# Performance work log

Measured on AMD Instinct MI355X. Metric: run time of the kernel, lower is better.

Reference implementation:

```python
import jax, jax.numpy as jnp
import numpy as np

EMBED_DIM = 64  # scale factor dim (matches head dim)


def setup_inputs() -> dict:
    key0 = jax.random.key(0)
    kq, kk, kv = jax.random.split(key0, 3)
    shape = (2, 16, 2048, 64)  # [B, H, S, D]
    return {
        "query": jax.random.normal(kq, shape, dtype=jnp.float32),
        "key": jax.random.normal(kk, shape, dtype=jnp.float32),
        "value": jax.random.normal(kv, shape, dtype=jnp.float32),
    }


def reference(query, key, value):
    # qk = Q K^T / sqrt(embed_dim); softmax over last dim; @ V
    inv_scale = jnp.sqrt(jnp.asarray(EMBED_DIM, dtype=query.dtype))
    scores = jnp.einsum("bhqd,bhkd->bhqk", query, key) / inv_scale
    probs = jax.nn.softmax(scores, axis=-1)
    # dropout_p=0.0 -> identity (eval semantics)
    return jnp.einsum("bhqk,bhkd->bhqd", probs, value)
```

## Files before the change

kernel.cpp:

```cpp
#include <hip/hip_runtime.h>
#include <hip/hip_bf16.h>

#define S_LEN 2048
#define DDIM  64
#define NT    (S_LEN / 64)
#define SCALE  0.125f
#define SCALE2 0.18033688f
#define NELEM  4194304
#define NQROW  65536
#define WC_LGKM0 0xc07f

#if __has_builtin(__builtin_amdgcn_permlane32_swap) && __has_builtin(__builtin_amdgcn_permlane16_swap)
#define HAVE_PLSWAP 1
#else
#define HAVE_PLSWAP 0
#endif

typedef __attribute__((ext_vector_type(8))) short short8;
typedef __attribute__((ext_vector_type(4))) float floatx4;
typedef __attribute__((ext_vector_type(2))) float floatx2;
typedef __attribute__((ext_vector_type(2))) __bf16 bf16x2;

__device__ __forceinline__ short f2bf(float f) {
    union { float f; unsigned u; } v; v.f = f;
    return (short)((v.u + 0x7fffu + ((v.u >> 16) & 1u)) >> 16);
}

__device__ __forceinline__ unsigned pk2bf(float a, float b) {
    floatx2 f; f[0] = a; f[1] = b;
    bf16x2 h = __builtin_convertvector(f, bf16x2);
    union { bf16x2 v; unsigned u; } c; c.v = h; return c.u;
}

__device__ __forceinline__ float fexp2(float x) {
#if __has_builtin(__builtin_amdgcn_exp2f)
    return __builtin_amdgcn_exp2f(x);
#else
    return exp2f(x);
#endif
}

#if HAVE_PLSWAP
__device__ __forceinline__ void plswap32(unsigned &a, unsigned &b) {
    auto r = __builtin_amdgcn_permlane32_swap((int)a, (int)b, false, false);
    a = (unsigned)r[0]; b = (unsigned)r[1];
}
__device__ __forceinline__ void plswap16(unsigned &a, unsigned &b) {
    auto r = __builtin_amdgcn_permlane16_swap((int)a, (int)b, false, false);
    a = (unsigned)r[0]; b = (unsigned)r[1];
}
#endif

__global__ __launch_bounds__(256) void prep_kv(const float* __restrict__ K,
                                               const float* __restrict__ V,
                                               short* __restrict__ Kb,
                                               short* __restrict__ Vt) {
    const int bh = blockIdx.x & 31;
    const int st = blockIdx.x >> 5;
    const int t  = threadIdx.x;
    const size_t tile_off = (size_t)bh * (S_LEN * DDIM) + (size_t)st * (64 * DDIM);

    {
        const float* src = K + tile_off + t * 16;
        short* dst = Kb + tile_off + t * 16;
        #pragma unroll
        for (int h = 0; h < 2; ++h) {
            float4 a = *(const float4*)(src + h * 8);
            float4 b = *(const float4*)(src + h * 8 + 4);
            uint4 o;
            o.x = pk2bf(a.x, a.y); o.y = pk2bf(a.z, a.w);
            o.z = pk2bf(b.x, b.y); o.w = pk2bf(b.z, b.w);
            *(uint4*)(dst + h * 8) = o;
        }
    }

    {
        const int s4 = (t & 15) * 4;
        const int d4 = (t >> 4) * 4;
        const float* src = V + tile_off;
        float4 v0 = *(const float4*)(src + (size_t)(s4 + 0) * 64 + d4);
        float4 v1 = *(const float4*)(src + (size_t)(s4 + 1) * 64 + d4);
        float4 v2 = *(const float4*)(src + (size_t)(s4 + 2) * 64 + d4);
        float4 v3 = *(const float4*)(src + (size_t)(s4 + 3) * 64 + d4);
        const float* r0 = (const float*)&v0;
        const float* r1 = (const float*)&v1;
        const float* r2 = (const float*)&v2;
        const float* r3 = (const float*)&v3;
        short* dstb = Vt + (size_t)bh * (DDIM * S_LEN) + (size_t)st * 64 + s4;
        #pragma unroll
        for (int dd = 0; dd < 4; ++dd) {
            uint2 o;
            o.x = pk2bf(r0[dd], r1[dd]);
            o.y = pk2bf(r2[dd], r3[dd]);
            *(uint2*)(dstb + (size_t)(d4 + dd) * S_LEN) = o;
        }
    }
}

__global__ __launch_bounds__(512) void attn_sm8(
    const float* __restrict__ Q, const short* __restrict__ Kb,
    const short* __restrict__ Vt, float* __restrict__ O)
{
    __shared__ short Ks[2][64 * 64];
    __shared__ short Vs[2][64 * 64];
    __shared__ float Dl[128];
#if !HAVE_PLSWAP
    __shared__ short Pl[8][32 * 64];
#endif

    constexpr int NIT = NT / 2;

    const int tid  = threadIdx.x;
    const int wave = tid >> 6;
    const int grp  = wave >> 2;
    const int w4   = wave & 3;
    const int lane = tid & 63;
    const int l16  = lane & 15;
    const int quad = lane >> 4;
    const int x7   = l16 & 7;

    const int bh = blockIdx.x & 31;
    const int qt = blockIdx.x >> 5;
    const int ks = grp;
    const size_t base = (size_t)bh * (S_LEN * DDIM);

    const int g   = tid & 255;
    const int ci0 = g,        r0 = ci0 >> 3, c0 = (ci0 & 7) ^ (r0 & 7);
    const int ci1 = 256 + g,  r1 = ci1 >> 3, c1 = (ci1 & 7) ^ (r1 & 7);
    const size_t koff = (size_t)ks * NIT * (64 * 64);
    const size_t voff = (size_t)ks * NIT * 64;
    const short* pK0 = Kb + base + koff + r0 * 64 + c0 * 8;
    const short* pK1 = Kb + base + koff + r1 * 64 + c1 * 8;
    const short* pV0 = Vt + base + voff + (size_t)r0 * S_LEN + c0 * 8;
    const short* pV1 = Vt + base + voff + (size_t)r1 * S_LEN + c1 * 8;

    short8 rk0 = *(const short8*)pK0;
    short8 rk1 = *(const short8*)pK1;
    short8 rv0 = *(const short8*)pV0;
    short8 rv1 = *(const short8*)pV1;

    short8 qf[2][2];
    #pragma unroll
    for (int nq = 0; nq < 2; ++nq) {
        const float* qp = Q + base + (size_t)(qt * 128 + w4 * 32 + nq * 16 + l16) * 64 + quad * 8;
        #pragma unroll
        for (int kt = 0; kt < 2; ++kt) {
            float4 a = *(const float4*)(qp + kt * 32);
            float4 b = *(const float4*)(qp + kt * 32 + 4);
            union { unsigned u[4]; short8 s; } qc;
            qc.u[0] = pk2bf(a.x * SCALE2, a.y * SCALE2);
            qc.u[1] = pk2bf(a.z * SCALE2, a.w * SCALE2);
            qc.u[2] = pk2bf(b.x * SCALE2, b.y * SCALE2);
            qc.u[3] = pk2bf(b.z * SCALE2, b.w * SCALE2);
            qf[nq][kt] = qc.s;
        }
    }

    floatx4 oacc[2][4];
    float rs[2];
    #pragma unroll
    for (int mt = 0; mt < 2; ++mt) {
        #pragma unroll
        for (int dt = 0; dt < 4; ++dt) oacc[mt][dt] = (floatx4){0.f,0.f,0.f,0.f};
        rs[mt] = 0.f;
    }

    short* Ksg = &Ks[grp][0];
    short* Vsg = &Vs[grp][0];
#if !HAVE_PLSWAP
    short* Pw = &Pl[wave][0];
#endif

    for (int kb = 0; kb < NIT; ++kb) {
        if (kb) __builtin_amdgcn_s_barrier();

        *(short8*)&Ksg[ci0 * 8] = rk0;
        *(short8*)&Ksg[ci1 * 8] = rk1;
        *(short8*)&Vsg[ci0 * 8] = rv0;
        *(short8*)&Vsg[ci1 * 8] = rv1;

        if (kb + 1 < NIT) {
            const int ok = (kb + 1) * (64 * 64), ov = (kb + 1) * 64;
            rk0 = *(const short8*)(pK0 + ok);
            rk1 = *(const short8*)(pK1 + ok);
            rv0 = *(const short8*)(pV0 + ov);
            rv1 = *(const short8*)(pV1 + ov);
        }

        __builtin_amdgcn_s_waitcnt(WC_LGKM0);
        __builtin_amdgcn_s_barrier();

        floatx4 sc[2][4];
        #pragma unroll
        for (int mk = 0; mk < 4; ++mk) {
            floatx4 a0 = (floatx4){0.f,0.f,0.f,0.f};
            floatx4 a1 = (floatx4){0.f,0.f,0.f,0.f};
            #pragma unroll
            for (int kt = 0; kt < 2; ++kt) {
                const int csw = (kt * 4 + quad) ^ x7;
                short8 kf = *(const short8*)&Ksg[(mk * 16 + l16) * 64 + csw * 8];
                a0 = __builtin_amdgcn_mfma_f32_16x16x32_bf16(kf, qf[0][kt], a0, 0, 0, 0);
                a1 = __builtin_amdgcn_mfma_f32_16x16x32_bf16(kf, qf[1][kt], a1, 0, 0, 0);
            }
            sc[0][mk] = a0; sc[1][mk] = a1;
        }

#if HAVE_PLSWAP
        unsigned pa[2][4], pb[2][4];
        #pragma unroll
        for (int nq = 0; nq < 2; ++nq) {
            #pragma unroll
            for (int mk = 0; mk < 4; ++mk) {
                float p0 = fexp2(sc[nq][mk][0]);
                float p1 = fexp2(sc[nq][mk][1]);
                float p2 = fexp2(sc[nq][mk][2]);
                float p3 = fexp2(sc[nq][mk][3]);
                rs[nq] += (p0 + p1) + (p2 + p3);
                pa[nq][mk] = pk2bf(p0, p1);
                pb[nq][mk] = pk2bf(p2, p3);
            }
        }

        #pragma unroll
        for (int kt = 0; kt < 2; ++kt) {
            short8 pf[2];
            #pragma unroll
            for (int nq = 0; nq < 2; ++nq) {
                unsigned a0 = pa[nq][2 * kt], a1 = pa[nq][2 * kt + 1];
                unsigned b0 = pb[nq][2 * kt], b1 = pb[nq][2 * kt + 1];
                plswap32(a0, a1); plswap16(a0, a1);
                plswap32(b0, b1); plswap16(b0, b1);
                union { unsigned u[4]; short8 s; } c;
                c.u[0] = a0; c.u[1] = b0; c.u[2] = a1; c.u[3] = b1;
                pf[nq] = c.s;
            }
            const int csw = (kt * 4 + quad) ^ x7;
            #pragma unroll
            for (int dt = 0; dt < 4; ++dt) {
                short8 vf = *(const short8*)&Vsg[(dt * 16 + l16) * 64 + csw * 8];
                oacc[0][dt] = __builtin_amdgcn_mfma_f32_16x16x32_bf16(pf[0], vf, oacc[0][dt], 0, 0, 0);
                oacc[1][dt] = __builtin_amdgcn_mfma_f32_16x16x32_bf16(pf[1], vf, oacc[1][dt], 0, 0, 0);
            }
        }
#else
        #pragma unroll
        for (int nq = 0; nq < 2; ++nq) {
            const int prow = (nq * 16 + l16) * 64;
            #pragma unroll
            for (int mk = 0; mk < 4; ++mk) {
                float p0 = fexp2(sc[nq][mk][0]);
                float p1 = fexp2(sc[nq][mk][1]);
                float p2 = fexp2(sc[nq][mk][2]);
                float p3 = fexp2(sc[nq][mk][3]);
                rs[nq] += (p0 + p1) + (p2 + p3);
                uint2 pv; pv.x = pk2bf(p0, p1); pv.y = pk2bf(p2, p3);
                const int c8 = (mk * 4 + quad) ^ (2 * x7);
                *(uint2*)&Pw[prow + c8 * 4] = pv;
            }
        }
        #pragma unroll
        for (int kt = 0; kt < 2; ++kt) {
            const int csw = (kt * 4 + quad) ^ x7;
            short8 pf0 = *(const short8*)&Pw[(l16)      * 64 + csw * 8];
            short8 pf1 = *(const short8*)&Pw[(16 + l16) * 64 + csw * 8];
            #pragma unroll
            for (int dt = 0; dt < 4; ++dt) {
                short8 vf = *(const short8*)&Vsg[(dt * 16 + l16) * 64 + csw * 8];
                oacc[0][dt] = __builtin_amdgcn_mfma_f32_16x16x32_bf16(pf0, vf, oacc[0][dt], 0, 0, 0);
                oacc[1][dt] = __builtin_amdgcn_mfma_f32_16x16x32_bf16(pf1, vf, oacc[1][dt], 0, 0, 0);
            }
        }
#endif
    }

    float sred[2];
    #pragma unroll
    for (int nq = 0; nq < 2; ++nq) {
        float s = rs[nq];
        s += __shfl_xor(s, 16, 64);
        s += __shfl_xor(s, 32, 64);
        sred[nq] = s;
    }

    if (grp == 1 && quad == 0) {
        Dl[w4 * 32 + l16]      = sred[0];
        Dl[w4 * 32 + 16 + l16] = sred[1];
    }
    __syncthreads();

    float invt[2];
    if (grp == 0) {
        invt[0] = 1.0f / (sred[0] + Dl[w4 * 32 + l16]);
        invt[1] = 1.0f / (sred[1] + Dl[w4 * 32 + 16 + l16]);
    }

    float* Nb = (float*)&Ks[0][0];
    #pragma unroll
    for (int mt = 0; mt < 2; ++mt) {
        if (grp == 1) {
            #pragma unroll
            for (int dt = 0; dt < 4; ++dt)
                #pragma unroll
                for (int r = 0; r < 4; ++r)
                    Nb[(dt * 4 + r) * 256 + w4 * 64 + lane] = oacc[mt][dt][r];
        }
        __syncthreads();
        if (grp == 0) {
            #pragma unroll
            for (int r = 0; r < 4; ++r) {
                const int row = qt * 128 + w4 * 32 + mt * 16 + quad * 4 + r;
                const float it = __shfl(invt[mt], quad * 4 + r, 64);
                float* op = O + base + (size_t)row * 64 + l16;
                #pragma unroll
                for (int dt = 0; dt < 4; ++dt)
                    op[dt * 16] = (oacc[mt][dt][r] + Nb[(dt * 4 + r) * 256 + w4 * 64 + lane]) * it;
            }
        }
        __syncthreads();
    }
}

#define BQ    64
#define BKEY  64
#define KPAD  72

__global__ __launch_bounds__(256) void attn_kernel(
    const float* __restrict__ Q, const float* __restrict__ K,
    const float* __restrict__ V, float* __restrict__ O)
{
    __shared__ short Ksh[BKEY * KPAD];
    __shared__ short Vtt[DDIM * KPAD];
    __shared__ short Pls[4][16 * KPAD];

    const int tid  = threadIdx.x;
    const int wave = tid >> 6;
    const int lane = tid & 63;
    const int l16  = lane & 15;
    const int quad = lane >> 4;

    const int bh = blockIdx.x & 31;
    const int qt = blockIdx.x >> 5;
    const size_t base = (size_t)bh * S_LEN * DDIM;

    const int qrow = qt * BQ + wave * 16 + l16;
    short8 qf[2];
    {
        const float* qp = Q + base + (size_t)qrow * DDIM + quad * 8;
        #pragma unroll
        for (int kt = 0; kt < 2; ++kt) {
            float4 a = *(const float4*)(qp + kt * 32);
            float4 b = *(const float4*)(qp + kt * 32 + 4);
            short* d = (short*)&qf[kt];
            d[0]=f2bf(a.x*SCALE); d[1]=f2bf(a.y*SCALE); d[2]=f2bf(a.z*SCALE); d[3]=f2bf(a.w*SCALE);
            d[4]=f2bf(b.x*SCALE); d[5]=f2bf(b.y*SCALE); d[6]=f2bf(b.z*SCALE); d[7]=f2bf(b.w*SCALE);
        }
    }

    float m_i[4], l_i[4];
    floatx4 oacc[4];
    #pragma unroll
    for (int r = 0; r < 4; ++r) { m_i[r] = -3.0e38f; l_i[r] = 0.f; }
    #pragma unroll
    for (int dt = 0; dt < 4; ++dt) oacc[dt] = (floatx4){0.f, 0.f, 0.f, 0.f};

    const int skey = tid >> 2;
    const int scol = (tid & 3) * 4;

    for (int kb = 0; kb < S_LEN / BKEY; ++kb) {
        const float* Kg = K + base + (size_t)kb * BKEY * DDIM + (size_t)skey * DDIM;
        const float* Vg = V + base + (size_t)kb * BKEY * DDIM + (size_t)skey * DDIM;
        #pragma unroll
        for (int i = 0; i < 4; ++i) {
            const int c = scol + i * 16;
            float4 kv = *(const float4*)(Kg + c);
            short* kd = &Ksh[skey * KPAD + c];
            kd[0]=f2bf(kv.x); kd[1]=f2bf(kv.y); kd[2]=f2bf(kv.z); kd[3]=f2bf(kv.w);
            float4 vv = *(const float4*)(Vg + c);
            Vtt[(c+0)*KPAD + skey] = f2bf(vv.x);
            Vtt[(c+1)*KPAD + skey] = f2bf(vv.y);
            Vtt[(c+2)*KPAD + skey] = f2bf(vv.z);
            Vtt[(c+3)*KPAD + skey] = f2bf(vv.w);
        }
        __syncthreads();

        floatx4 sc[4];
        #pragma unroll
        for (int nt = 0; nt < 4; ++nt) {
            floatx4 acc = (floatx4){0.f, 0.f, 0.f, 0.f};
            #pragma unroll
            for (int kt = 0; kt < 2; ++kt) {
                short8 kf = *(const short8*)&Ksh[(nt*16 + l16) * KPAD + kt*32 + quad*8];
                acc = __builtin_amdgcn_mfma_f32_16x16x32_bf16(qf[kt], kf, acc, 0, 0, 0);
            }
            sc[nt] = acc;
        }

        short* Pw = &Pls[wave][0];
        #pragma unroll
        for (int r = 0; r < 4; ++r) {
            float mx = fmaxf(fmaxf(sc[0][r], sc[1][r]), fmaxf(sc[2][r], sc[3][r]));
            #pragma unroll
            for (int off = 1; off < 16; off <<= 1)
                mx = fmaxf(mx, __shfl_xor(mx, off, 64));
            const float mnew  = fmaxf(m_i[r], mx);
            const float alpha = __expf(m_i[r] - mnew);
            m_i[r] = mnew;
            float rsum = 0.f;
            #pragma unroll
            for (int nt = 0; nt < 4; ++nt) {
                float p = __expf(sc[nt][r] - mnew);
                rsum += p;
                Pw[(quad*4 + r) * KPAD + nt*16 + l16] = f2bf(p);
            }
            #pragma unroll
            for (int off = 1; off < 16; off <<= 1)
                rsum += __shfl_xor(rsum, off, 64);
            l_i[r] = l_i[r] * alpha + rsum;
            oacc[0][r] *= alpha; oacc[1][r] *= alpha;
            oacc[2][r] *= alpha; oacc[3][r] *= alpha;
        }

        #pragma unroll
        for (int kt = 0; kt < 2; ++kt) {
            short8 pf = *(const short8*)&Pw[l16 * KPAD + kt*32 + quad*8];
            #pragma unroll
            for (int dt = 0; dt < 4; ++dt) {
                short8 vf = *(const short8*)&Vtt[(dt*16 + l16) * KPAD + kt*32 + quad*8];
                oacc[dt] = __builtin_amdgcn_mfma_f32_16x16x32_bf16(pf, vf, oacc[dt], 0, 0, 0);
            }
        }
        __syncthreads();
    }

    #pragma unroll
    for (int r = 0; r < 4; ++r) {
        const float inv = 1.0f / l_i[r];
        const int row = qt * BQ + wave * 16 + quad * 4 + r;
        float* op = O + base + (size_t)row * DDIM + l16;
        #pragma unroll
        for (int dt = 0; dt < 4; ++dt)
            op[dt * 16] = oacc[dt][r] * inv;
    }
}

extern "C" void kernel_launch(void* const* d_in, const int* in_sizes, int n_in,
                              void* d_out, int out_size, void* d_ws, size_t ws_size,
                              hipStream_t stream) {
    const float* Q = (const float*)d_in[0];
    const float* K = (const float*)d_in[1];
    const float* V = (const float*)d_in[2];
    float* O = (float*)d_out;

    const size_t prep_bytes = (size_t)NELEM * 2 * 2;

    if (ws_size >= prep_bytes) {
        short* Kb  = (short*)d_ws;
        short* Vtp = (short*)d_ws + NELEM;
        prep_kv<<<dim3(1024), dim3(256), 0, stream>>>(K, V, Kb, Vtp);
        attn_sm8<<<dim3(512), dim3(512), 0, stream>>>(Q, Kb, Vtp, O);
    } else {
        attn_kernel<<<dim3(1024), dim3(256), 0, stream>>>(Q, K, V, O);
    }
}
```

Measured before the change: 138.2 us.

## Fuse K/V bf16 conversion and V transpose into the attention kernel

Removes the separate prep_kv pass that converted K and V to bf16 (with V transposed) in a workspace. The attention kernel now loads fp32 K/V tiles directly, converts them in registers, and writes V transposed into swizzled shared memory. This saves a kernel launch and a round trip of bf16 K/V through global memory. In exchange each block re-converts K/V and issues twice as many global load bytes per tile, and the V transpose writes to LDS become scattered. The fallback kernel and the non-permlane path are also dropped.

```diff
diff --git a/kernel.cpp b/kernel.cpp
--- a/kernel.cpp
+++ b/kernel.cpp
@@ -4,27 +4,13 @@
 #define S_LEN 2048
 #define DDIM  64
 #define NT    (S_LEN / 64)
-#define SCALE  0.125f
 #define SCALE2 0.18033688f
-#define NELEM  4194304
-#define NQROW  65536
 #define WC_LGKM0 0xc07f
-
-#if __has_builtin(__builtin_amdgcn_permlane32_swap) && __has_builtin(__builtin_amdgcn_permlane16_swap)
-#define HAVE_PLSWAP 1
-#else
-#define HAVE_PLSWAP 0
-#endif
 
 typedef __attribute__((ext_vector_type(8))) short short8;
 typedef __attribute__((ext_vector_type(4))) float floatx4;
 typedef __attribute__((ext_vector_type(2))) float floatx2;
 typedef __attribute__((ext_vector_type(2))) __bf16 bf16x2;
-
-__device__ __forceinline__ short f2bf(float f) {
-    union { float f; unsigned u; } v; v.f = f;
-    return (short)((v.u + 0x7fffu + ((v.u >> 16) & 1u)) >> 16);
-}
 
 __device__ __forceinline__ unsigned pk2bf(float a, float b) {
     floatx2 f; f[0] = a; f[1] = b;
@@ -40,7 +26,6 @@
 #endif
 }
 
-#if HAVE_PLSWAP
 __device__ __forceinline__ void plswap32(unsigned &a, unsigned &b) {
     auto r = __builtin_amdgcn_permlane32_swap((int)a, (int)b, false, false);
     a = (unsigned)r[0]; b = (unsigned)r[1];
@@ -49,64 +34,14 @@
     auto r = __builtin_amdgcn_permlane16_swap((int)a, (int)b, false, false);
     a = (unsigned)r[0]; b = (unsigned)r[1];
 }
-#endif
-
-__global__ __launch_bounds__(256) void prep_kv(const float* __restrict__ K,
-                                               const float* __restrict__ V,
-                                               short* __restrict__ Kb,
-                                               short* __restrict__ Vt) {
-    const int bh = blockIdx.x & 31;
-    const int st = blockIdx.x >> 5;
-    const int t  = threadIdx.x;
-    const size_t tile_off = (size_t)bh * (S_LEN * DDIM) + (size_t)st * (64 * DDIM);
-
-    {
-        const float* src = K + tile_off + t * 16;
-        short* dst = Kb + tile_off + t * 16;
-        #pragma unroll
-        for (int h = 0; h < 2; ++h) {
-            float4 a = *(const float4*)(src + h * 8);
-            float4 b = *(const float4*)(src + h * 8 + 4);
-            uint4 o;
-            o.x = pk2bf(a.x, a.y); o.y = pk2bf(a.z, a.w);
-            o.z = pk2bf(b.x, b.y); o.w = pk2bf(b.z, b.w);
-            *(uint4*)(dst + h * 8) = o;
-        }
-    }
-
-    {
-        const int s4 = (t & 15) * 4;
-        const int d4 = (t >> 4) * 4;
-        const float* src = V + tile_off;
-        float4 v0 = *(const float4*)(src + (size_t)(s4 + 0) * 64 + d4);
-        float4 v1 = *(const float4*)(src + (size_t)(s4 + 1) * 64 + d4);
-        float4 v2 = *(const float4*)(src + (size_t)(s4 + 2) * 64 + d4);
-        float4 v3 = *(const float4*)(src + (size_t)(s4 + 3) * 64 + d4);
-        const float* r0 = (const float*)&v0;
-        const float* r1 = (const float*)&v1;
-        const float* r2 = (const float*)&v2;
-        const float* r3 = (const float*)&v3;
-        short* dstb = Vt + (size_t)bh * (DDIM * S_LEN) + (size_t)st * 64 + s4;
-        #pragma unroll
-        for (int dd = 0; dd < 4; ++dd) {
-            uint2 o;
-            o.x = pk2bf(r0[dd], r1[dd]);
-            o.y = pk2bf(r2[dd], r3[dd]);
-            *(uint2*)(dstb + (size_t)(d4 + dd) * S_LEN) = o;
-        }
-    }
-}
-
-__global__ __launch_bounds__(512) void attn_sm8(
-    const float* __restrict__ Q, const short* __restrict__ Kb,
-    const short* __restrict__ Vt, float* __restrict__ O)
+
+__global__ __launch_bounds__(512) void attn_fused(
+    const float* __restrict__ Q, const float* __restrict__ K,
+    const float* __restrict__ V, float* __restrict__ O)
 {
     __shared__ short Ks[2][64 * 64];
     __shared__ short Vs[2][64 * 64];
     __shared__ float Dl[128];
-#if !HAVE_PLSWAP
-    __shared__ short Pl[8][32 * 64];
-#endif
 
     constexpr int NIT = NT / 2;
 
@@ -121,23 +56,51 @@
 
     const int bh = blockIdx.x & 31;
     const int qt = blockIdx.x >> 5;
-    const int ks = grp;
     const size_t base = (size_t)bh * (S_LEN * DDIM);
 
     const int g   = tid & 255;
     const int ci0 = g,        r0 = ci0 >> 3, c0 = (ci0 & 7) ^ (r0 & 7);
     const int ci1 = 256 + g,  r1 = ci1 >> 3, c1 = (ci1 & 7) ^ (r1 & 7);
-    const size_t koff = (size_t)ks * NIT * (64 * 64);
-    const size_t voff = (size_t)ks * NIT * 64;
-    const short* pK0 = Kb + base + koff + r0 * 64 + c0 * 8;
-    const short* pK1 = Kb + base + koff + r1 * 64 + c1 * 8;
-    const short* pV0 = Vt + base + voff + (size_t)r0 * S_LEN + c0 * 8;
-    const short* pV1 = Vt + base + voff + (size_t)r1 * S_LEN + c1 * 8;
-
-    short8 rk0 = *(const short8*)pK0;
-    short8 rk1 = *(const short8*)pK1;
-    short8 rv0 = *(const short8*)pV0;
-    short8 rv1 = *(const short8*)pV1;
+    const int s4 = (g & 15) * 4;
+    const int d4 = (g >> 4) * 4;
+
+    const size_t koff = (size_t)grp * NIT * (64 * 64);
+    const float* pK0 = K + base + koff + r0 * 64 + c0 * 8;
+    const float* pK1 = K + base + koff + r1 * 64 + c1 * 8;
+    const float* pV  = V + base + koff + (size_t)s4 * 64 + d4;
+
+    short* Ksg = &Ks[grp][0];
+    short* Vsg = &Vs[grp][0];
+
+    float4 ka0 = *(const float4*)(pK0);
+    float4 ka1 = *(const float4*)(pK0 + 4);
+    float4 kc0 = *(const float4*)(pK1);
+    float4 kc1 = *(const float4*)(pK1 + 4);
+    float4 va  = *(const float4*)(pV);
+    float4 vb  = *(const float4*)(pV + 64);
+    float4 vc  = *(const float4*)(pV + 128);
+    float4 vd  = *(const float4*)(pV + 192);
+
+#define STAGE_WRITE() do {                                                    \
+    uint4 ow0, ow1;                                                           \
+    ow0.x = pk2bf(ka0.x, ka0.y); ow0.y = pk2bf(ka0.z, ka0.w);                 \
+    ow0.z = pk2bf(ka1.x, ka1.y); ow0.w = pk2bf(ka1.z, ka1.w);                 \
+    ow1.x = pk2bf(kc0.x, kc0.y); ow1.y = pk2bf(kc0.z, kc0.w);                 \
+    ow1.z = pk2bf(kc1.x, kc1.y); ow1.w = pk2bf(kc1.z, kc1.w);                 \
+    *(uint4*)&Ksg[ci0 * 8] = ow0;                                             \
+    *(uint4*)&Ksg[ci1 * 8] = ow1;                                             \
+    const float* f0 = (const float*)&va; const float* f1 = (const float*)&vb; \
+    const float* f2 = (const float*)&vc; const float* f3 = (const float*)&vd; \
+    _Pragma("unroll")                                                         \
+    for (int dd = 0; dd < 4; ++dd) {                                          \
+        uint2 ov;                                                             \
+        ov.x = pk2bf(f0[dd], f1[dd]);                                         \
+        ov.y = pk2bf(f2[dd], f3[dd]);                                         \
+        const int rr = d4 + dd;                                               \
+        const int sc = (s4 >> 3) ^ (rr & 7);                                  \
+        *(uint2*)&Vsg[rr * 64 + sc * 8 + (s4 & 7)] = ov;                      \
+    }                                                                         \
+} while (0)
 
     short8 qf[2][2];
     #pragma unroll
@@ -165,26 +128,21 @@
         rs[mt] = 0.f;
     }
 
-    short* Ksg = &Ks[grp][0];
-    short* Vsg = &Vs[grp][0];
-#if !HAVE_PLSWAP
-    short* Pw = &Pl[wave][0];
-#endif
-
     for (int kb = 0; kb < NIT; ++kb) {
         if (kb) __builtin_amdgcn_s_barrier();
 
-        *(short8*)&Ksg[ci0 * 8] = rk0;
-        *(short8*)&Ksg[ci1 * 8] = rk1;
-        *(short8*)&Vsg[ci0 * 8] = rv0;
-        *(short8*)&Vsg[ci1 * 8] = rv1;
+        STAGE_WRITE();
 
         if (kb + 1 < NIT) {
-            const int ok = (kb + 1) * (64 * 64), ov = (kb + 1) * 64;
-            rk0 = *(const short8*)(pK0 + ok);
-            rk1 = *(const short8*)(pK1 + ok);
-            rv0 = *(const short8*)(pV0 + ov);
-            rv1 = *(const short8*)(pV1 + ov);
+            const int ot = (kb + 1) * 4096;
+            ka0 = *(const float4*)(pK0 + ot);
+            ka1 = *(const float4*)(pK0 + ot + 4);
+            kc0 = *(const float4*)(pK1 + ot);
+            kc1 = *(const float4*)(pK1 + ot + 4);
+            va  = *(const float4*)(pV + ot);
+            vb  = *(const float4*)(pV + ot + 64);
+            vc  = *(const float4*)(pV + ot + 128);
+            vd  = *(const float4*)(pV + ot + 192);
         }
 
         __builtin_amdgcn_s_waitcnt(WC_LGKM0);
@@ -205,7 +163,6 @@
             sc[0][mk] = a0; sc[1][mk] = a1;
         }
 
-#if HAVE_PLSWAP
         unsigned pa[2][4], pb[2][4];
         #pragma unroll
         for (int nq = 0; nq < 2; ++nq) {
@@ -242,35 +199,6 @@
                 oacc[1][dt] = __builtin_amdgcn_mfma_f32_16x16x32_bf16(pf[1], vf, oacc[1][dt], 0, 0, 0);
             }
         }
-#else
-        #pragma unroll
-        for (int nq = 0; nq < 2; ++nq) {
-            const int prow = (nq * 16 + l16) * 64;
-            #pragma unroll
-            for (int mk = 0; mk < 4; ++mk) {
-                float p0 = fexp2(sc[nq][mk][0]);
-                float p1 = fexp2(sc[nq][mk][1]);
-                float p2 = fexp2(sc[nq][mk][2]);
-                float p3 = fexp2(sc[nq][mk][3]);
-                rs[nq] += (p0 + p1) + (p2 + p3);
-                uint2 pv; pv.x = pk2bf(p0, p1); pv.y = pk2bf(p2, p3);
-                const int c8 = (mk * 4 + quad) ^ (2 * x7);
-                *(uint2*)&Pw[prow + c8 * 4] = pv;
-            }
-        }
-        #pragma unroll
-        for (int kt = 0; kt < 2; ++kt) {
-            const int csw = (kt * 4 + quad) ^ x7;
-            short8 pf0 = *(const short8*)&Pw[(l16)      * 64 + csw * 8];
-            short8 pf1 = *(const short8*)&Pw[(16 + l16) * 64 + csw * 8];
-            #pragma unroll
-            for (int dt = 0; dt < 4; ++dt) {
-                short8 vf = *(const short8*)&Vsg[(dt * 16 + l16) * 64 + csw * 8];
-                oacc[0][dt] = __builtin_amdgcn_mfma_f32_16x16x32_bf16(pf0, vf, oacc[0][dt], 0, 0, 0);
-                oacc[1][dt] = __builtin_amdgcn_mfma_f32_16x16x32_bf16(pf1, vf, oacc[1][dt], 0, 0, 0);
-            }
-        }
-#endif
     }
 
     float sred[2];
@@ -318,129 +246,7 @@
         }
         __syncthreads();
     }
-}
-
-#define BQ    64
-#define BKEY  64
-#define KPAD  72
-
-__global__ __launch_bounds__(256) void attn_kernel(
-    const float* __restrict__ Q, const float* __restrict__ K,
-    const float* __restrict__ V, float* __restrict__ O)
-{
-    __shared__ short Ksh[BKEY * KPAD];
-    __shared__ short Vtt[DDIM * KPAD];
-    __shared__ short Pls[4][16 * KPAD];
-
-    const int tid  = threadIdx.x;
-    const int wave = tid >> 6;
-    const int lane = tid & 63;
-    const int l16  = lane & 15;
-    const int quad = lane >> 4;
-
-    const int bh = blockIdx.x & 31;
-    const int qt = blockIdx.x >> 5;
-    const size_t base = (size_t)bh * S_LEN * DDIM;
-
-    const int qrow = qt * BQ + wave * 16 + l16;
-    short8 qf[2];
-    {
-        const float* qp = Q + base + (size_t)qrow * DDIM + quad * 8;
-        #pragma unroll
-        for (int kt = 0; kt < 2; ++kt) {
-            float4 a = *(const float4*)(qp + kt * 32);
-            float4 b = *(const float4*)(qp + kt * 32 + 4);
-            short* d = (short*)&qf[kt];
-            d[0]=f2bf(a.x*SCALE); d[1]=f2bf(a.y*SCALE); d[2]=f2bf(a.z*SCALE); d[3]=f2bf(a.w*SCALE);
-            d[4]=f2bf(b.x*SCALE); d[5]=f2bf(b.y*SCALE); d[6]=f2bf(b.z*SCALE); d[7]=f2bf(b.w*SCALE);
-        }
-    }
-
-    float m_i[4], l_i[4];
-    floatx4 oacc[4];
-    #pragma unroll
-    for (int r = 0; r < 4; ++r) { m_i[r] = -3.0e38f; l_i[r] = 0.f; }
-    #pragma unroll
-    for (int dt = 0; dt < 4; ++dt) oacc[dt] = (floatx4){0.f, 0.f, 0.f, 0.f};
-
-    const int skey = tid >> 2;
-    const int scol = (tid & 3) * 4;
-
-    for (int kb = 0; kb < S_LEN / BKEY; ++kb) {
-        const float* Kg = K + base + (size_t)kb * BKEY * DDIM + (size_t)skey * DDIM;
-        const float* Vg = V + base + (size_t)kb * BKEY * DDIM + (size_t)skey * DDIM;
-        #pragma unroll
-        for (int i = 0; i < 4; ++i) {
-            const int c = scol + i * 16;
-            float4 kv = *(const float4*)(Kg + c);
-            short* kd = &Ksh[skey * KPAD + c];
-            kd[0]=f2bf(kv.x); kd[1]=f2bf(kv.y); kd[2]=f2bf(kv.z); kd[3]=f2bf(kv.w);
-            float4 vv = *(const float4*)(Vg + c);
-            Vtt[(c+0)*KPAD + skey] = f2bf(vv.x);
-            Vtt[(c+1)*KPAD + skey] = f2bf(vv.y);
-            Vtt[(c+2)*KPAD + skey] = f2bf(vv.z);
-            Vtt[(c+3)*KPAD + skey] = f2bf(vv.w);
-        }
-        __syncthreads();
-
-        floatx4 sc[4];
-        #pragma unroll
-        for (int nt = 0; nt < 4; ++nt) {
-            floatx4 acc = (floatx4){0.f, 0.f, 0.f, 0.f};
-            #pragma unroll
-            for (int kt = 0; kt < 2; ++kt) {
-                short8 kf = *(const short8*)&Ksh[(nt*16 + l16) * KPAD + kt*32 + quad*8];
-                acc = __builtin_amdgcn_mfma_f32_16x16x32_bf16(qf[kt], kf, acc, 0, 0, 0);
-            }
-            sc[nt] = acc;
-        }
-
-        short* Pw = &Pls[wave][0];
-        #pragma unroll
-        for (int r = 0; r < 4; ++r) {
-            float mx = fmaxf(fmaxf(sc[0][r], sc[1][r]), fmaxf(sc[2][r], sc[3][r]));
-            #pragma unroll
-            for (int off = 1; off < 16; off <<= 1)
-                mx = fmaxf(mx, __shfl_xor(mx, off, 64));
-            const float mnew  = fmaxf(m_i[r], mx);
-            const float alpha = __expf(m_i[r] - mnew);
-            m_i[r] = mnew;
-            float rsum = 0.f;
-            #pragma unroll
-            for (int nt = 0; nt < 4; ++nt) {
-                float p = __expf(sc[nt][r] - mnew);
-                rsum += p;
-                Pw[(quad*4 + r) * KPAD + nt*16 + l16] = f2bf(p);
-            }
-            #pragma unroll
-            for (int off = 1; off < 16; off <<= 1)
-                rsum += __shfl_xor(rsum, off, 64);
-            l_i[r] = l_i[r] * alpha + rsum;
-            oacc[0][r] *= alpha; oacc[1][r] *= alpha;
-            oacc[2][r] *= alpha; oacc[3][r] *= alpha;
-        }
-
-        #pragma unroll
-        for (int kt = 0; kt < 2; ++kt) {
-            short8 pf = *(const short8*)&Pw[l16 * KPAD + kt*32 + quad*8];
-            #pragma unroll
-            for (int dt = 0; dt < 4; ++dt) {
-                short8 vf = *(const short8*)&Vtt[(dt*16 + l16) * KPAD + kt*32 + quad*8];
-                oacc[dt] = __builtin_amdgcn_mfma_f32_16x16x32_bf16(pf, vf, oacc[dt], 0, 0, 0);
-            }
-        }
-        __syncthreads();
-    }
-
-    #pragma unroll
-    for (int r = 0; r < 4; ++r) {
-        const float inv = 1.0f / l_i[r];
-        const int row = qt * BQ + wave * 16 + quad * 4 + r;
-        float* op = O + base + (size_t)row * DDIM + l16;
-        #pragma unroll
-        for (int dt = 0; dt < 4; ++dt)
-            op[dt * 16] = oacc[dt][r] * inv;
-    }
+#undef STAGE_WRITE
 }
 
 extern "C" void kernel_launch(void* const* d_in, const int* in_sizes, int n_in,
@@ -450,15 +256,7 @@
     const float* K = (const float*)d_in[1];
     const float* V = (const float*)d_in[2];
     float* O = (float*)d_out;
-
-    const size_t prep_bytes = (size_t)NELEM * 2 * 2;
-
-    if (ws_size >= prep_bytes) {
-        short* Kb  = (short*)d_ws;
-        short* Vtp = (short*)d_ws + NELEM;
-        prep_kv<<<dim3(1024), dim3(256), 0, stream>>>(K, V, Kb, Vtp);
-        attn_sm8<<<dim3(512), dim3(512), 0, stream>>>(Q, Kb, Vtp, O);
-    } else {
-        attn_kernel<<<dim3(1024), dim3(256), 0, stream>>>(Q, K, V, O);
-    }
-}
+    (void)d_ws; (void)ws_size;
+
+    attn_fused<<<dim3(512), dim3(512), 0, stream>>>(Q, K, V, O);
+}
```

Measured after the change: 140.0 us. No clear change (+1.4%).
